# Optimization experiments

Measured on AMD Instinct MI355X. Metric: run time of the kernel, lower is better.

## Reference

```python
import jax, jax.numpy as jnp
import numpy as np

N_NODES = 50000
N_EDGES = 800000
F_IN = 64
F_OUT = 64
SELF_LOOP_W = 2.0  # GCNConv improved=True


def setup_inputs() -> dict:
    key = jax.random.key(0)
    k1, k2, k3 = jax.random.split(key, 3)
    x = jax.random.normal(k1, (N_NODES, F_IN), dtype=jnp.float32)
    edge_index = jax.random.randint(k2, (2, N_EDGES), 0, N_NODES, dtype=jnp.int64)
    W = jax.random.normal(k3, (F_IN, F_OUT), dtype=jnp.float32) / np.sqrt(F_IN)
    b = jnp.zeros((F_OUT,), dtype=jnp.float32)
    return {"x": x, "edge_index": edge_index, "W": W, "b": b}


def reference(x, edge_index, W, b):
    N = x.shape[0]
    E = edge_index.shape[1]
    src, dst = edge_index[0], edge_index[1]
    # add self loops with weight 2.0 (improved=True)
    loop = jnp.arange(N, dtype=src.dtype)
    src_f = jnp.concatenate([src, loop])
    dst_f = jnp.concatenate([dst, loop])
    w_edge = jnp.concatenate([jnp.ones((E,), x.dtype), jnp.full((N,), SELF_LOOP_W, x.dtype)])
    # symmetric normalization: deg over target nodes (PyG gcn_norm)
    deg = jax.ops.segment_sum(w_edge, dst_f, num_segments=N)
    dinv = jnp.where(deg > 0, deg ** -0.5, 0.0)
    norm = dinv[src_f] * w_edge * dinv[dst_f]  # [E+N]
    # dense transform, then gather-scale-scatter
    h = x @ W  # [N, F_OUT]
    agg = jax.ops.segment_sum(norm[:, None] * h[src_f], dst_f, num_segments=N)
    out = jax.nn.relu(agg + b)
    return jax.nn.log_softmax(out, axis=1)
```

## Files before the change

kernel.cpp:

```cpp
#include <hip/hip_runtime.h>
#include <hip/hip_fp16.h>

#define N_NODES 50000
#define N_EDGES 800000
#define F 64
#define NB ((N_NODES + 255) / 256)
#define NBUCK 391
#define BSHIFT 7
#define BMASK 127
#define BCAP 3072
#define P1_BLOCKS ((N_EDGES + 1023) / 1024)
#define NPB 32

typedef __attribute__((ext_vector_type(2))) float f32x2;


union H2U { __half2 h; unsigned u; };

__global__ void k_init(int* __restrict__ bcur) {
    int t = blockIdx.x * blockDim.x + threadIdx.x;
    if (t < NBUCK) bcur[t] = 0;
}

__global__ __launch_bounds__(1024) void k_p1c(const int* __restrict__ src,
                                              const int* __restrict__ dst,
                                              int* __restrict__ bcur,
                                              int* __restrict__ staging,
                                              const float4* __restrict__ x4,
                                              unsigned* __restrict__ xq) {
    __shared__ int lcnt[NBUCK];
    __shared__ int lbase[NBUCK];
    int t = threadIdx.x;
    int g = blockIdx.x * 1024 + t;
    if (t < NBUCK) lcnt[t] = 0;
    if (g < N_NODES * (F / 4)) {
        float4 v = x4[g];
        unsigned w = 0;
        w = __builtin_amdgcn_cvt_pk_fp8_f32(v.x, v.y, w, false);
        w = __builtin_amdgcn_cvt_pk_fp8_f32(v.z, v.w, w, true);
        xq[g] = w;
    }
    __syncthreads();
    int s = 0, d = 0, bk = 0, rank = 0;
    bool valid = (g < N_EDGES);
    if (valid) {
        s = src[g]; d = dst[g];
        bk = d >> BSHIFT;
        rank = atomicAdd(&lcnt[bk], 1);
    }
    __syncthreads();
    if (t < NBUCK && lcnt[t]) lbase[t] = atomicAdd(&bcur[t], lcnt[t]);
    __syncthreads();
    if (valid)
        staging[bk * BCAP + lbase[bk] + rank] = ((d & BMASK) << 16) | s;
}

__global__ __launch_bounds__(512) void k_p23(const int* __restrict__ staging,
                                             const int* __restrict__ bcur,
                                             int* __restrict__ offsets,
                                             int* __restrict__ counts,
                                             float* __restrict__ dinv,
                                             int* __restrict__ pack) {
    __shared__ int ncnt[128];
    __shared__ int lcur[128];
    int t = threadIdx.x;
    int b = blockIdx.x;
    int nb0 = b << BSHIFT;
    if (t < 128) ncnt[t] = 0;
    __syncthreads();
    int beg = b * BCAP, end = beg + bcur[b];
    for (int i = beg + t; i < end; i += 512)
        atomicAdd(&ncnt[staging[i] >> 16], 1);
    __syncthreads();
    int c = (t < 128) ? ncnt[t] : 0;
    for (int off = 1; off < 128; off <<= 1) {
        int u = (t < 128 && t >= off) ? ncnt[t - off] : 0;
        __syncthreads();
        if (t < 128) ncnt[t] += u;
        __syncthreads();
    }
    if (t < 128) {
        int goff = beg + (ncnt[t] - c);
        lcur[t] = goff;
        int node = nb0 + t;
        if (node < N_NODES) {
            offsets[node] = goff;
            counts[node]  = c;
            dinv[node]    = rsqrtf((float)c + 2.0f);
        }
    }
    __syncthreads();
    for (int i = beg + t; i < end; i += 512) {
        int v = staging[i];
        int pos = atomicAdd(&lcur[v >> 16], 1);
        pack[pos] = v & 0xFFFF;
    }
}

__global__ __launch_bounds__(512) void k_agg(const unsigned* __restrict__ xq,
                                             const float* __restrict__ dinv,
                                             const int* __restrict__ offsets,
                                             const int* __restrict__ counts,
                                             const int* __restrict__ pack,
                                             const float* __restrict__ W,
                                             const float* __restrict__ bias,
                                             float* __restrict__ out) {
    __shared__ unsigned sWu[F * F / 2];
    __shared__ float srow[NPB][F];
    int t = threadIdx.x;
    for (int i = t; i < F * F / 2; i += 512) {
        int p = i >> 6, c = i & 63;
        H2U u;
        u.h = __float22half2_rn(make_float2(W[(2 * p) * F + c], W[(2 * p + 1) * F + c]));
        sWu[i] = u.u;
    }
    __syncthreads();

    int wid = t >> 6, lane = t & 63;
    int qe = lane >> 4, qc = lane & 15;
    int nbase = blockIdx.x * NPB + wid * 4;

    int4   off4 = *reinterpret_cast<const int4*>(offsets + nbase);
    int4   cnt4 = *reinterpret_cast<const int4*>(counts + nbase);
    float4 dv4  = *reinterpret_cast<const float4*>(dinv + nbase);
    int   begs[4] = { off4.x, off4.y, off4.z, off4.w };
    int   degs[4] = { cnt4.x, cnt4.y, cnt4.z, cnt4.w };
    float dns[4]  = { dv4.x, dv4.y, dv4.z, dv4.w };
#pragma unroll
    for (int i = 0; i < 4; ++i)
        if (nbase + i >= N_NODES) { degs[i] = 0; dns[i] = 0.f; begs[i] = 0; }

    int pls[4]; float nms[4];
#pragma unroll
    for (int i = 0; i < 4; ++i) {
        int s = 0; float nm = 0.f;
        if (lane < degs[i]) {
            s = pack[begs[i] + lane];
            nm = dns[i] * dinv[s];
        }
        pls[i] = s; nms[i] = nm;
    }

#pragma unroll
    for (int i = 0; i < 4; i += 2) {
        float a00 = 0.f, a01 = 0.f, a02 = 0.f, a03 = 0.f;
        float a10 = 0.f, a11 = 0.f, a12 = 0.f, a13 = 0.f;
        int lim = min(max(degs[i], degs[i + 1]), 64);
        for (int r = 0; r < lim; r += 8) {
            int e0 = r + qe, e1 = r + 4 + qe;
            int   s00 = __shfl(pls[i], e0);     float m00 = __shfl(nms[i], e0);
            int   s01 = __shfl(pls[i], e1);     float m01 = __shfl(nms[i], e1);
            int   s10 = __shfl(pls[i + 1], e0); float m10 = __shfl(nms[i + 1], e0);
            int   s11 = __shfl(pls[i + 1], e1); float m11 = __shfl(nms[i + 1], e1);
            unsigned q00 = xq[(size_t)s00 * 16 + qc];
            unsigned q01 = xq[(size_t)s01 * 16 + qc];
            unsigned q10 = xq[(size_t)s10 * 16 + qc];
            unsigned q11 = xq[(size_t)s11 * 16 + qc];
            f32x2 f;
            f = __builtin_amdgcn_cvt_pk_f32_fp8(q00, false);
            a00 = fmaf(m00, f.x, a00); a01 = fmaf(m00, f.y, a01);
            f = __builtin_amdgcn_cvt_pk_f32_fp8(q00, true);
            a02 = fmaf(m00, f.x, a02); a03 = fmaf(m00, f.y, a03);
            f = __builtin_amdgcn_cvt_pk_f32_fp8(q01, false);
            a00 = fmaf(m01, f.x, a00); a01 = fmaf(m01, f.y, a01);
            f = __builtin_amdgcn_cvt_pk_f32_fp8(q01, true);
            a02 = fmaf(m01, f.x, a02); a03 = fmaf(m01, f.y, a03);
            f = __builtin_amdgcn_cvt_pk_f32_fp8(q10, false);
            a10 = fmaf(m10, f.x, a10); a11 = fmaf(m10, f.y, a11);
            f = __builtin_amdgcn_cvt_pk_f32_fp8(q10, true);
            a12 = fmaf(m10, f.x, a12); a13 = fmaf(m10, f.y, a13);
            f = __builtin_amdgcn_cvt_pk_f32_fp8(q11, false);
            a10 = fmaf(m11, f.x, a10); a11 = fmaf(m11, f.y, a11);
            f = __builtin_amdgcn_cvt_pk_f32_fp8(q11, true);
            a12 = fmaf(m11, f.x, a12); a13 = fmaf(m11, f.y, a13);
        }
#pragma unroll
        for (int k = 0; k < 2; ++k) {
            int dend = begs[i + k] + degs[i + k];
            for (int base = begs[i + k] + 64; base < dend; base += 8) {
                int e0o = base + qe, e1o = base + 4 + qe;
                int s0 = 0, s1 = 0; float m0 = 0.f, m1 = 0.f;
                if (e0o < dend) { s0 = pack[e0o]; m0 = dns[i + k] * dinv[s0]; }
                if (e1o < dend) { s1 = pack[e1o]; m1 = dns[i + k] * dinv[s1]; }
                unsigned q0 = xq[(size_t)s0 * 16 + qc];
                unsigned q1 = xq[(size_t)s1 * 16 + qc];
                float* A = (k == 0) ? &a00 : &a10;
                f32x2 f;
                f = __builtin_amdgcn_cvt_pk_f32_fp8(q0, false);
                A[0] = fmaf(m0, f.x, A[0]); A[1] = fmaf(m0, f.y, A[1]);
                f = __builtin_amdgcn_cvt_pk_f32_fp8(q0, true);
                A[2] = fmaf(m0, f.x, A[2]); A[3] = fmaf(m0, f.y, A[3]);
                f = __builtin_amdgcn_cvt_pk_f32_fp8(q1, false);
                A[0] = fmaf(m1, f.x, A[0]); A[1] = fmaf(m1, f.y, A[1]);
                f = __builtin_amdgcn_cvt_pk_f32_fp8(q1, true);
                A[2] = fmaf(m1, f.x, A[2]); A[3] = fmaf(m1, f.y, A[3]);
            }
        }
        a00 += __shfl_xor(a00, 16); a10 += __shfl_xor(a10, 16);
        a01 += __shfl_xor(a01, 16); a11 += __shfl_xor(a11, 16);
        a02 += __shfl_xor(a02, 16); a12 += __shfl_xor(a12, 16);
        a03 += __shfl_xor(a03, 16); a13 += __shfl_xor(a13, 16);
        a00 += __shfl_xor(a00, 32); a10 += __shfl_xor(a10, 32);
        a01 += __shfl_xor(a01, 32); a11 += __shfl_xor(a11, 32);
        a02 += __shfl_xor(a02, 32); a12 += __shfl_xor(a12, 32);
        a03 += __shfl_xor(a03, 32); a13 += __shfl_xor(a13, 32);
        if (qe == 0) {
            int n0 = nbase + i;
            if (n0 < N_NODES) {
                float c2 = 2.0f * dns[i] * dns[i];
                unsigned q = xq[(size_t)n0 * 16 + qc];
                f32x2 f0 = __builtin_amdgcn_cvt_pk_f32_fp8(q, false);
                f32x2 f1 = __builtin_amdgcn_cvt_pk_f32_fp8(q, true);
                float4 w;
                w.x = fmaf(c2, f0.x, a00); w.y = fmaf(c2, f0.y, a01);
                w.z = fmaf(c2, f1.x, a02); w.w = fmaf(c2, f1.y, a03);
                *reinterpret_cast<float4*>(&srow[wid * 4 + i][qc * 4]) = w;
            }
            int n1 = nbase + i + 1;
            if (n1 < N_NODES) {
                float c2 = 2.0f * dns[i + 1] * dns[i + 1];
                unsigned q = xq[(size_t)n1 * 16 + qc];
                f32x2 f0 = __builtin_amdgcn_cvt_pk_f32_fp8(q, false);
                f32x2 f1 = __builtin_amdgcn_cvt_pk_f32_fp8(q, true);
                float4 w;
                w.x = fmaf(c2, f0.x, a10); w.y = fmaf(c2, f0.y, a11);
                w.z = fmaf(c2, f1.x, a12); w.w = fmaf(c2, f1.y, a13);
                *reinterpret_cast<float4*>(&srow[wid * 4 + i + 1][qc * 4]) = w;
            }
        }
    }

    asm volatile("s_waitcnt lgkmcnt(0)" ::: "memory");

    float bl = bias[lane];
    float y0 = bl, y1 = bl, y2 = bl, y3 = bl;
#pragma unroll 4
    for (int j = 0; j < 16; ++j) {
        float4 r0 = *reinterpret_cast<const float4*>(&srow[wid * 4 + 0][j * 4]);
        float4 r1 = *reinterpret_cast<const float4*>(&srow[wid * 4 + 1][j * 4]);
        float4 r2 = *reinterpret_cast<const float4*>(&srow[wid * 4 + 2][j * 4]);
        float4 r3 = *reinterpret_cast<const float4*>(&srow[wid * 4 + 3][j * 4]);
        H2U ua, ub;
        ua.u = sWu[(2 * j) * F + lane];
        ub.u = sWu[(2 * j + 1) * F + lane];
        float2 wab = __half22float2(ua.h);
        float2 wcd = __half22float2(ub.h);
        y0 = fmaf(r0.x, wab.x, y0); y0 = fmaf(r0.y, wab.y, y0); y0 = fmaf(r0.z, wcd.x, y0); y0 = fmaf(r0.w, wcd.y, y0);
        y1 = fmaf(r1.x, wab.x, y1); y1 = fmaf(r1.y, wab.y, y1); y1 = fmaf(r1.z, wcd.x, y1); y1 = fmaf(r1.w, wcd.y, y1);
        y2 = fmaf(r2.x, wab.x, y2); y2 = fmaf(r2.y, wab.y, y2); y2 = fmaf(r2.z, wcd.x, y2); y2 = fmaf(r2.w, wcd.y, y2);
        y3 = fmaf(r3.x, wab.x, y3); y3 = fmaf(r3.y, wab.y, y3); y3 = fmaf(r3.z, wcd.x, y3); y3 = fmaf(r3.w, wcd.y, y3);
    }

    float ys[4] = { y0, y1, y2, y3 };
#pragma unroll
    for (int i = 0; i < 4; ++i) {
        float y = fmaxf(ys[i], 0.0f);
        float mx = y;
#pragma unroll
        for (int off = 32; off > 0; off >>= 1)
            mx = fmaxf(mx, __shfl_xor(mx, off));
        float ex = __expf(y - mx);
        float ss = ex;
#pragma unroll
        for (int off = 32; off > 0; off >>= 1)
            ss += __shfl_xor(ss, off);
        int n = nbase + i;
        if (n < N_NODES) out[n * F + lane] = y - mx - __logf(ss);
    }
}


__global__ void k_count_b(const int* __restrict__ dst, int* __restrict__ counts) {
    int e = blockIdx.x * blockDim.x + threadIdx.x;
    if (e < N_EDGES) atomicAdd(&counts[dst[e]], 1);
}
__global__ __launch_bounds__(256) void k_blocksum(const int* __restrict__ counts,
                                                  int* __restrict__ bs) {
    __shared__ int sh[256];
    int t = threadIdx.x;
    int g = blockIdx.x * 256 + t;
    int v = (g < N_NODES) ? counts[g] : 0;
    sh[t] = v;
    __syncthreads();
    for (int off = 128; off > 0; off >>= 1) {
        if (t < off) sh[t] += sh[t + off];
        __syncthreads();
    }
    if (t == 0) bs[blockIdx.x] = sh[0];
}
__global__ __launch_bounds__(256) void k_scanblocks(int* __restrict__ bs) {
    __shared__ int sh[256];
    int t = threadIdx.x;
    int v = (t < NB) ? bs[t] : 0;
    sh[t] = v;
    __syncthreads();
    for (int off = 1; off < 256; off <<= 1) {
        int u = (t >= off) ? sh[t - off] : 0;
        __syncthreads();
        sh[t] += u;
        __syncthreads();
    }
    if (t < NB) bs[t] = sh[t] - v;
}
__global__ __launch_bounds__(256) void k_offsets_b(int* __restrict__ counts,
                                                   const int* __restrict__ bs,
                                                   int* __restrict__ offsets,
                                                   float* __restrict__ dinv) {
    __shared__ int sh[256];
    int t = threadIdx.x;
    int g = blockIdx.x * 256 + t;
    int c = (g < N_NODES) ? counts[g] : 0;
    sh[t] = c;
    __syncthreads();
    for (int off = 1; off < 256; off <<= 1) {
        int u = (t >= off) ? sh[t - off] : 0;
        __syncthreads();
        sh[t] += u;
        __syncthreads();
    }
    int excl = sh[t] - c + bs[blockIdx.x];
    if (g < N_NODES) {
        offsets[g] = excl;
        counts[g]  = excl;
        dinv[g]    = rsqrtf((float)c + 2.0f);
    }
    if (g == 0) offsets[N_NODES] = N_EDGES;
}
__global__ void k_fill_b(const int* __restrict__ src, const int* __restrict__ dst,
                         int* __restrict__ cursor, int* __restrict__ sorted_src) {
    int e = blockIdx.x * blockDim.x + threadIdx.x;
    if (e < N_EDGES) {
        int pos = atomicAdd(&cursor[dst[e]], 1);
        sorted_src[pos] = src[e];
    }
}
__global__ __launch_bounds__(256) void k_agg_b(const float* __restrict__ x,
                                               const float* __restrict__ dinv,
                                               const int* __restrict__ offsets,
                                               const int* __restrict__ sorted_src,
                                               const float* __restrict__ W,
                                               const float* __restrict__ b,
                                               float* __restrict__ out) {
    __shared__ float sW[F * F];
    __shared__ float srow[4][F];
    int t = threadIdx.x;
    for (int i = t; i < F * F; i += 256) sW[i] = W[i];
    int wid = t >> 6, lane = t & 63;
    int n = blockIdx.x * 4 + wid;
    int qe = lane >> 4, qc = lane & 15;
    float dn = dinv[n];
    int beg = offsets[n], end = offsets[n + 1];
    float4 acc = make_float4(0.f, 0.f, 0.f, 0.f);
    for (int base = beg; base < end; base += 4) {
        int e = base + qe;
        int s = n; float nm = 0.f;
        if (e < end) { s = sorted_src[e]; nm = dn * dinv[s]; }
        float4 v = reinterpret_cast<const float4*>(x + (size_t)s * F)[qc];
        acc.x = fmaf(nm, v.x, acc.x); acc.y = fmaf(nm, v.y, acc.y);
        acc.z = fmaf(nm, v.z, acc.z); acc.w = fmaf(nm, v.w, acc.w);
    }
    acc.x += __shfl_xor(acc.x, 16); acc.y += __shfl_xor(acc.y, 16);
    acc.z += __shfl_xor(acc.z, 16); acc.w += __shfl_xor(acc.w, 16);
    acc.x += __shfl_xor(acc.x, 32); acc.y += __shfl_xor(acc.y, 32);
    acc.z += __shfl_xor(acc.z, 32); acc.w += __shfl_xor(acc.w, 32);
    float c2 = 2.0f * dn * dn;
    float4 xv = reinterpret_cast<const float4*>(x + (size_t)n * F)[qc];
    acc.x = fmaf(c2, xv.x, acc.x); acc.y = fmaf(c2, xv.y, acc.y);
    acc.z = fmaf(c2, xv.z, acc.z); acc.w = fmaf(c2, xv.w, acc.w);
    if (qe == 0) reinterpret_cast<float4*>(&srow[wid][0])[qc] = acc;
    __syncthreads();
    float y = b[lane];
#pragma unroll
    for (int k = 0; k < F; ++k) y = fmaf(srow[wid][k], sW[k * F + lane], y);
    y = fmaxf(y, 0.0f);
    float m = y;
#pragma unroll
    for (int off = 32; off > 0; off >>= 1) m = fmaxf(m, __shfl_xor(m, off));
    float ex = __expf(y - m);
    float ss = ex;
#pragma unroll
    for (int off = 32; off > 0; off >>= 1) ss += __shfl_xor(ss, off);
    out[n * F + lane] = y - m - __logf(ss);
}


__global__ void k_init_deg_f(float* __restrict__ deg) {
    int i = blockIdx.x * blockDim.x + threadIdx.x;
    if (i < N_NODES) deg[i] = 2.0f;
}
__global__ void k_count_f(const int* __restrict__ dst, float* __restrict__ deg) {
    int e = blockIdx.x * blockDim.x + threadIdx.x;
    if (e < N_EDGES) atomicAdd(&deg[dst[e]], 1.0f);
}
__global__ void k_dinv_f(float* __restrict__ deg) {
    int i = blockIdx.x * blockDim.x + threadIdx.x;
    if (i < N_NODES) deg[i] = rsqrtf(deg[i]);
}
__global__ void k_selfinit_f(const float* __restrict__ x, const float* __restrict__ dinv,
                             float* __restrict__ agg) {
    int t = blockIdx.x * blockDim.x + threadIdx.x;
    if (t >= N_NODES * (F / 4)) return;
    int n = t >> 4;
    float d = dinv[n];
    float c = 2.0f * d * d;
    float4 v = reinterpret_cast<const float4*>(x)[t];
    float4 o; o.x = c*v.x; o.y = c*v.y; o.z = c*v.z; o.w = c*v.w;
    reinterpret_cast<float4*>(agg)[t] = o;
}
__global__ __launch_bounds__(256) void k_scatter_f(const int* __restrict__ src,
                                                   const int* __restrict__ dst,
                                                   const float* __restrict__ x,
                                                   const float* __restrict__ dinv,
                                                   float* __restrict__ agg) {
    int wave = (blockIdx.x * blockDim.x + threadIdx.x) >> 6;
    int lane = threadIdx.x & 63;
    if (wave >= N_EDGES) return;
    int s = src[wave], d = dst[wave];
    atomicAdd(&agg[d * F + lane], dinv[s] * dinv[d] * x[s * F + lane]);
}
__global__ __launch_bounds__(256) void k_final_f(const float* __restrict__ W,
                                                 const float* __restrict__ b,
                                                 float* __restrict__ out) {
    __shared__ float sW[F * F];
    __shared__ float srow[4][F];
    int t = threadIdx.x;
    for (int i = t; i < F * F; i += 256) sW[i] = W[i];
    int wid = t >> 6, lane = t & 63;
    int n = blockIdx.x * 4 + wid;
    float rv = out[n * F + lane];
    srow[wid][lane] = rv;
    __syncthreads();
    float y = b[lane];
#pragma unroll
    for (int k = 0; k < F; ++k) y = fmaf(srow[wid][k], sW[k * F + lane], y);
    y = fmaxf(y, 0.0f);
    float m = y;
#pragma unroll
    for (int off = 32; off > 0; off >>= 1) m = fmaxf(m, __shfl_xor(m, off));
    float ex = __expf(y - m);
    float ss = ex;
#pragma unroll
    for (int off = 32; off > 0; off >>= 1) ss += __shfl_xor(ss, off);
    out[n * F + lane] = y - m - __logf(ss);
}


extern "C" void kernel_launch(void* const* d_in, const int* in_sizes, int n_in,
                              void* d_out, int out_size, void* d_ws, size_t ws_size,
                              hipStream_t stream) {
    const float* x    = (const float*)d_in[0];
    const int*   eidx = (const int*)d_in[1];
    const float* W    = (const float*)d_in[2];
    const float* b    = (const float*)d_in[3];
    const int* src = eidx;
    const int* dst = eidx + N_EDGES;
    float* out = (float*)d_out;

    const size_t NEED_A12 = 8618112;
    const size_t NEED_B   = 3801040;

    if (ws_size >= NEED_A12) {
        char* ws = (char*)d_ws;
        int*      offsets = (int*)(ws);
        int*      counts  = (int*)(ws + 200064);
        float*    dinv    = (float*)(ws + 400128);
        int*      bcur    = (int*)(ws + 600192);
        int*      pack    = (int*)(ws + 601792);
        unsigned* xq      = (unsigned*)(ws + 5418112);
        int*      staging = (int*)d_out;

        k_init<<<1, 512, 0, stream>>>(bcur);
        k_p1c<<<P1_BLOCKS, 1024, 0, stream>>>(src, dst, bcur, staging,
                                              (const float4*)x, xq);
        k_p23<<<NBUCK, 512, 0, stream>>>(staging, bcur, offsets, counts, dinv, pack);
        k_agg<<<(N_NODES + NPB - 1) / NPB, 512, 0, stream>>>(
            xq, dinv, offsets, counts, pack, W, b, out);
    } else if (ws_size >= NEED_B) {
        char* ws = (char*)d_ws;
        int*   counts     = (int*)(ws);
        int*   offsets    = (int*)(ws + 200000);
        float* dinv       = (float*)(ws + 400016);
        int*   bs         = (int*)(ws + 600016);
        int*   sorted_src = (int*)(ws + 601040);

        hipMemsetAsync(counts, 0, N_NODES * sizeof(int), stream);
        k_count_b<<<(N_EDGES + 255) / 256, 256, 0, stream>>>(dst, counts);
        k_blocksum<<<NB, 256, 0, stream>>>(counts, bs);
        k_scanblocks<<<1, 256, 0, stream>>>(bs);
        k_offsets_b<<<NB, 256, 0, stream>>>(counts, bs, offsets, dinv);
        k_fill_b<<<(N_EDGES + 255) / 256, 256, 0, stream>>>(src, dst, counts, sorted_src);
        k_agg_b<<<N_NODES / 4, 256, 0, stream>>>(x, dinv, offsets, sorted_src, W, b, out);
    } else {
        float* deg = (float*)d_ws;
        k_init_deg_f<<<(N_NODES + 255) / 256, 256, 0, stream>>>(deg);
        k_count_f<<<(N_EDGES + 255) / 256, 256, 0, stream>>>(dst, deg);
        k_dinv_f<<<(N_NODES + 255) / 256, 256, 0, stream>>>(deg);
        k_selfinit_f<<<(N_NODES * (F / 4) + 255) / 256, 256, 0, stream>>>(x, deg, out);
        k_scatter_f<<<(N_EDGES * 64 + 255) / 256, 256, 0, stream>>>(src, dst, x, deg, out);
        k_final_f<<<N_NODES / 4, 256, 0, stream>>>(W, b, out);
    }
}
```

Baseline: 74.79 us.

## Precompute fp16 edge norms into CSR pack and simplify aggregation loop

New measurement: 78.46 us. 1.05x slower.

```diff
diff --git a/kernel.cpp b/kernel.cpp
--- a/kernel.cpp
+++ b/kernel.cpp
@@ -55,14 +55,12 @@
         staging[bk * BCAP + lbase[bk] + rank] = ((d & BMASK) << 16) | s;
 }
 
-__global__ __launch_bounds__(512) void k_p23(const int* __restrict__ staging,
-                                             const int* __restrict__ bcur,
-                                             int* __restrict__ offsets,
-                                             int* __restrict__ counts,
-                                             float* __restrict__ dinv,
-                                             int* __restrict__ pack) {
+__global__ __launch_bounds__(512) void k_p2(const int* __restrict__ staging,
+                                            const int* __restrict__ bcur,
+                                            int* __restrict__ offsets,
+                                            int* __restrict__ counts,
+                                            float* __restrict__ dinv) {
     __shared__ int ncnt[128];
-    __shared__ int lcur[128];
     int t = threadIdx.x;
     int b = blockIdx.x;
     int nb0 = b << BSHIFT;
@@ -80,20 +78,40 @@
         __syncthreads();
     }
     if (t < 128) {
-        int goff = beg + (ncnt[t] - c);
-        lcur[t] = goff;
         int node = nb0 + t;
         if (node < N_NODES) {
-            offsets[node] = goff;
+            offsets[node] = beg + (ncnt[t] - c);
             counts[node]  = c;
             dinv[node]    = rsqrtf((float)c + 2.0f);
         }
     }
-    __syncthreads();
+}
+
+__global__ __launch_bounds__(512) void k_p3(const int* __restrict__ staging,
+                                            const int* __restrict__ bcur,
+                                            const int* __restrict__ offsets,
+                                            const float* __restrict__ dinv,
+                                            unsigned* __restrict__ pack) {
+    __shared__ int lcur[128];
+    __shared__ float sdinv[128];
+    int t = threadIdx.x;
+    int b = blockIdx.x;
+    int nb0 = b << BSHIFT;
+    if (t < 128) {
+        int node = nb0 + t;
+        lcur[t]  = (node < N_NODES) ? offsets[node] : 0;
+        sdinv[t] = (node < N_NODES) ? dinv[node] : 0.f;
+    }
+    __syncthreads();
+    int beg = b * BCAP, end = beg + bcur[b];
     for (int i = beg + t; i < end; i += 512) {
         int v = staging[i];
-        int pos = atomicAdd(&lcur[v >> 16], 1);
-        pack[pos] = v & 0xFFFF;
+        int dl = v >> 16;
+        int s  = v & 0xFFFF;
+        int pos = atomicAdd(&lcur[dl], 1);
+        float nm = dinv[s] * sdinv[dl];
+        unsigned hv = (unsigned)__half_as_ushort(__float2half_rn(nm));
+        pack[pos] = (hv << 16) | (unsigned)s;
     }
 }
 
@@ -101,7 +119,7 @@
                                              const float* __restrict__ dinv,
                                              const int* __restrict__ offsets,
                                              const int* __restrict__ counts,
-                                             const int* __restrict__ pack,
+                                             const unsigned* __restrict__ pack,
                                              const float* __restrict__ W,
                                              const float* __restrict__ bias,
                                              float* __restrict__ out) {
@@ -130,71 +148,44 @@
     for (int i = 0; i < 4; ++i)
         if (nbase + i >= N_NODES) { degs[i] = 0; dns[i] = 0.f; begs[i] = 0; }
 
-    int pls[4]; float nms[4];
-#pragma unroll
-    for (int i = 0; i < 4; ++i) {
-        int s = 0; float nm = 0.f;
-        if (lane < degs[i]) {
-            s = pack[begs[i] + lane];
-            nm = dns[i] * dinv[s];
-        }
-        pls[i] = s; nms[i] = nm;
-    }
-
 #pragma unroll
     for (int i = 0; i < 4; i += 2) {
         float a00 = 0.f, a01 = 0.f, a02 = 0.f, a03 = 0.f;
         float a10 = 0.f, a11 = 0.f, a12 = 0.f, a13 = 0.f;
-        int lim = min(max(degs[i], degs[i + 1]), 64);
+        int dA = degs[i], dB = degs[i + 1];
+        int bA = begs[i], bB = begs[i + 1];
+        int lim = max(dA, dB);
         for (int r = 0; r < lim; r += 8) {
             int e0 = r + qe, e1 = r + 4 + qe;
-            int   s00 = __shfl(pls[i], e0);     float m00 = __shfl(nms[i], e0);
-            int   s01 = __shfl(pls[i], e1);     float m01 = __shfl(nms[i], e1);
-            int   s10 = __shfl(pls[i + 1], e0); float m10 = __shfl(nms[i + 1], e0);
-            int   s11 = __shfl(pls[i + 1], e1); float m11 = __shfl(nms[i + 1], e1);
-            unsigned q00 = xq[(size_t)s00 * 16 + qc];
-            unsigned q01 = xq[(size_t)s01 * 16 + qc];
-            unsigned q10 = xq[(size_t)s10 * 16 + qc];
-            unsigned q11 = xq[(size_t)s11 * 16 + qc];
+            unsigned pA0 = (e0 < dA) ? pack[bA + e0] : 0u;
+            unsigned pA1 = (e1 < dA) ? pack[bA + e1] : 0u;
+            unsigned pB0 = (e0 < dB) ? pack[bB + e0] : 0u;
+            unsigned pB1 = (e1 < dB) ? pack[bB + e1] : 0u;
+            unsigned qA0 = xq[(size_t)(pA0 & 0xFFFF) * 16 + qc];
+            unsigned qA1 = xq[(size_t)(pA1 & 0xFFFF) * 16 + qc];
+            unsigned qB0 = xq[(size_t)(pB0 & 0xFFFF) * 16 + qc];
+            unsigned qB1 = xq[(size_t)(pB1 & 0xFFFF) * 16 + qc];
+            float mA0 = __half2float(__ushort_as_half((unsigned short)(pA0 >> 16)));
+            float mA1 = __half2float(__ushort_as_half((unsigned short)(pA1 >> 16)));
+            float mB0 = __half2float(__ushort_as_half((unsigned short)(pB0 >> 16)));
+            float mB1 = __half2float(__ushort_as_half((unsigned short)(pB1 >> 16)));
             f32x2 f;
-            f = __builtin_amdgcn_cvt_pk_f32_fp8(q00, false);
-            a00 = fmaf(m00, f.x, a00); a01 = fmaf(m00, f.y, a01);
-            f = __builtin_amdgcn_cvt_pk_f32_fp8(q00, true);
-            a02 = fmaf(m00, f.x, a02); a03 = fmaf(m00, f.y, a03);
-            f = __builtin_amdgcn_cvt_pk_f32_fp8(q01, false);
-            a00 = fmaf(m01, f.x, a00); a01 = fmaf(m01, f.y, a01);
-            f = __builtin_amdgcn_cvt_pk_f32_fp8(q01, true);
-            a02 = fmaf(m01, f.x, a02); a03 = fmaf(m01, f.y, a03);
-            f = __builtin_amdgcn_cvt_pk_f32_fp8(q10, false);
-            a10 = fmaf(m10, f.x, a10); a11 = fmaf(m10, f.y, a11);
-            f = __builtin_amdgcn_cvt_pk_f32_fp8(q10, true);
-            a12 = fmaf(m10, f.x, a12); a13 = fmaf(m10, f.y, a13);
-            f = __builtin_amdgcn_cvt_pk_f32_fp8(q11, false);
-            a10 = fmaf(m11, f.x, a10); a11 = fmaf(m11, f.y, a11);
-            f = __builtin_amdgcn_cvt_pk_f32_fp8(q11, true);
-            a12 = fmaf(m11, f.x, a12); a13 = fmaf(m11, f.y, a13);
-        }
-#pragma unroll
-        for (int k = 0; k < 2; ++k) {
-            int dend = begs[i + k] + degs[i + k];
-            for (int base = begs[i + k] + 64; base < dend; base += 8) {
-                int e0o = base + qe, e1o = base + 4 + qe;
-                int s0 = 0, s1 = 0; float m0 = 0.f, m1 = 0.f;
-                if (e0o < dend) { s0 = pack[e0o]; m0 = dns[i + k] * dinv[s0]; }
-                if (e1o < dend) { s1 = pack[e1o]; m1 = dns[i + k] * dinv[s1]; }
-                unsigned q0 = xq[(size_t)s0 * 16 + qc];
-                unsigned q1 = xq[(size_t)s1 * 16 + qc];
-                float* A = (k == 0) ? &a00 : &a10;
-                f32x2 f;
-                f = __builtin_amdgcn_cvt_pk_f32_fp8(q0, false);
-                A[0] = fmaf(m0, f.x, A[0]); A[1] = fmaf(m0, f.y, A[1]);
-                f = __builtin_amdgcn_cvt_pk_f32_fp8(q0, true);
-                A[2] = fmaf(m0, f.x, A[2]); A[3] = fmaf(m0, f.y, A[3]);
-                f = __builtin_amdgcn_cvt_pk_f32_fp8(q1, false);
-                A[0] = fmaf(m1, f.x, A[0]); A[1] = fmaf(m1, f.y, A[1]);
-                f = __builtin_amdgcn_cvt_pk_f32_fp8(q1, true);
-                A[2] = fmaf(m1, f.x, A[2]); A[3] = fmaf(m1, f.y, A[3]);
-            }
+            f = __builtin_amdgcn_cvt_pk_f32_fp8(qA0, false);
+            a00 = fmaf(mA0, f.x, a00); a01 = fmaf(mA0, f.y, a01);
+            f = __builtin_amdgcn_cvt_pk_f32_fp8(qA0, true);
+            a02 = fmaf(mA0, f.x, a02); a03 = fmaf(mA0, f.y, a03);
+            f = __builtin_amdgcn_cvt_pk_f32_fp8(qA1, false);
+            a00 = fmaf(mA1, f.x, a00); a01 = fmaf(mA1, f.y, a01);
+            f = __builtin_amdgcn_cvt_pk_f32_fp8(qA1, true);
+            a02 = fmaf(mA1, f.x, a02); a03 = fmaf(mA1, f.y, a03);
+            f = __builtin_amdgcn_cvt_pk_f32_fp8(qB0, false);
+            a10 = fmaf(mB0, f.x, a10); a11 = fmaf(mB0, f.y, a11);
+            f = __builtin_amdgcn_cvt_pk_f32_fp8(qB0, true);
+            a12 = fmaf(mB0, f.x, a12); a13 = fmaf(mB0, f.y, a13);
+            f = __builtin_amdgcn_cvt_pk_f32_fp8(qB1, false);
+            a10 = fmaf(mB1, f.x, a10); a11 = fmaf(mB1, f.y, a11);
+            f = __builtin_amdgcn_cvt_pk_f32_fp8(qB1, true);
+            a12 = fmaf(mB1, f.x, a12); a13 = fmaf(mB1, f.y, a13);
         }
         a00 += __shfl_xor(a00, 16); a10 += __shfl_xor(a10, 16);
         a01 += __shfl_xor(a01, 16); a11 += __shfl_xor(a11, 16);
@@ -456,23 +447,24 @@
     const int* dst = eidx + N_EDGES;
     float* out = (float*)d_out;
 
-    const size_t NEED_A12 = 8618112;
+    const size_t NEED_A13 = 8618112;
     const size_t NEED_B   = 3801040;
 
-    if (ws_size >= NEED_A12) {
+    if (ws_size >= NEED_A13) {
         char* ws = (char*)d_ws;
         int*      offsets = (int*)(ws);
         int*      counts  = (int*)(ws + 200064);
         float*    dinv    = (float*)(ws + 400128);
         int*      bcur    = (int*)(ws + 600192);
-        int*      pack    = (int*)(ws + 601792);
+        unsigned* pack    = (unsigned*)(ws + 601792);
         unsigned* xq      = (unsigned*)(ws + 5418112);
         int*      staging = (int*)d_out;
 
         k_init<<<1, 512, 0, stream>>>(bcur);
         k_p1c<<<P1_BLOCKS, 1024, 0, stream>>>(src, dst, bcur, staging,
                                               (const float4*)x, xq);
-        k_p23<<<NBUCK, 512, 0, stream>>>(staging, bcur, offsets, counts, dinv, pack);
+        k_p2<<<NBUCK, 512, 0, stream>>>(staging, bcur, offsets, counts, dinv);
+        k_p3<<<NBUCK, 512, 0, stream>>>(staging, bcur, offsets, dinv, pack);
         k_agg<<<(N_NODES + NPB - 1) / NPB, 512, 0, stream>>>(
             xq, dinv, offsets, counts, pack, W, b, out);
     } else if (ws_size >= NEED_B) {
```
